# Performance work log

Measured on AMD Instinct MI355X. Metric: run time of the kernel, lower is better.

The kernel has to match this reference:

```python
import jax, jax.numpy as jnp
import numpy as np

EMBED = 512
HEADS = 8
DIM_HEAD = 64
SCALE = DIM_HEAD ** -0.5


def setup_inputs() -> dict:
    key = jax.random.key(0)
    k1, k2, k3 = jax.random.split(key, 3)
    x = jax.random.normal(k1, (1, EMBED, 64, 64), dtype=jnp.float32)
    # nn.Linear(embed, 3*embed) weight [out, in] -> store transposed [in, out] for x @ W
    W_qkv = jax.random.normal(k2, (EMBED, 3 * EMBED), dtype=jnp.float32) * (EMBED ** -0.5)
    b_qkv = jax.random.normal(k3, (3 * EMBED,), dtype=jnp.float32) * 0.01
    return {"x": x, "W_qkv": W_qkv, "b_qkv": b_qkv}


def reference(x, W_qkv, b_qkv):
    B, E, h, w = x.shape
    N = h * w
    # [B, E, H, W] -> [B, N, E]
    xs = x.reshape(B, E, N).transpose(0, 2, 1)
    qkv = xs @ W_qkv + b_qkv                      # [B, N, 3E]
    q, k, v = jnp.split(qkv, 3, axis=-1)          # each [B, N, E]

    def heads(t):
        return t.reshape(B, N, HEADS, DIM_HEAD).transpose(0, 2, 1, 3)  # [B, H, N, dh]

    q, k, v = heads(q), heads(k), heads(v)
    # raw (non-softmax) attention scores, materialized as in the original
    attn = jnp.einsum('bhqd,bhkd->bhqk', q, k) * SCALE  # [B, H, N, N]
    coarse_attn = attn.sum(axis=-2)                     # sum over queries -> [B, H, N]
    output = jnp.einsum('bhqk,bhkd->bhqd', attn, v)     # [B, H, N, dh]
    return coarse_attn, output
```

## Files before the change

### kernel.cpp

```cpp
#include <hip/hip_runtime.h>


#define N_TOK 4096
#define EMBED 512
#define J3    1536
#define HEADS 8
#define DH    64
#define SCALE 0.125f

typedef float  floatx4  __attribute__((ext_vector_type(4)));
typedef short  shortx8  __attribute__((ext_vector_type(8)));
typedef unsigned short ushortx4 __attribute__((ext_vector_type(4)));
typedef unsigned int u32;
typedef unsigned short ushort;

__device__ inline ushort f2bf(float f) {
    union { float f; u32 u; } x; x.f = f;
    u32 r = x.u + 0x7fffu + ((x.u >> 16) & 1u);
    return (ushort)(r >> 16);
}
__device__ inline float bf2f(ushort u) {
    union { u32 u; float f; } x; x.u = ((u32)u) << 16; return x.f;
}
__device__ static inline void async_copy16(void* lds, const void* g) {
    auto* gp = (const __attribute__((address_space(1))) u32*)g;
    auto* lp = (__attribute__((address_space(3))) u32*)lds;
    __builtin_amdgcn_global_load_lds(gp, lp, 16, 0, 0);
}
__device__ inline int permj(int j) {
    if (j < 512) return j;
    if (j < 1024) return 512 + ((j - 512) >> 6) * 128 + ((j - 512) & 63);
    return 512 + ((j - 1024) >> 6) * 128 + 64 + ((j - 1024) & 63);
}

__global__ __launch_bounds__(256) void prep(const float* __restrict__ x,
                                            const float* __restrict__ W,
                                            ushort* __restrict__ xT,
                                            ushort* __restrict__ WT,
                                            float* __restrict__ xsum) {
    const int t = threadIdx.x;
    int bx = blockIdx.x;
    const bool isx = bx < 64;
    const float* src = isx ? x : W;
    const int C = isx ? N_TOK : J3;
    if (!isx) bx -= 64;
    __shared__ float T[64][65];
    __shared__ float red[256];
    const int c0 = bx * 64, r0 = blockIdx.y * 64;
    #pragma unroll
    for (int k = 0; k < 16; ++k) {
        int i = t + 256 * k; int r = i >> 6, c = i & 63;
        T[r][c] = src[(size_t)(r0 + r) * C + c0 + c];
    }
    __syncthreads();
    if (isx) {
        int row = t >> 2, seg = (t & 3) * 16;
        float s = 0.f;
        #pragma unroll
        for (int cc = 0; cc < 16; ++cc) s += T[row][seg + cc];
        red[t] = s;
    }
    #pragma unroll
    for (int k = 0; k < 4; ++k) {
        int i = t + 256 * k; int cr = i >> 4, cc4 = (i & 15) * 4;
        ushortx4 o = { f2bf(T[cc4 + 0][cr]), f2bf(T[cc4 + 1][cr]),
                       f2bf(T[cc4 + 2][cr]), f2bf(T[cc4 + 3][cr]) };
        int dr = isx ? (c0 + cr) : permj(c0 + cr);
        ushort* dst = isx ? xT : WT;
        *(ushortx4*)&dst[(size_t)dr * 512 + r0 + cc4] = o;
    }
    if (isx) {
        __syncthreads();
        if ((t & 3) == 0)
            atomicAdd(&xsum[r0 + (t >> 2)], red[t] + red[t + 1] + red[t + 2] + red[t + 3]);
    }
}

__global__ __launch_bounds__(256) void qkv_m(const ushort* __restrict__ xT,
                                             const ushort* __restrict__ WT,
                                             const float* __restrict__ bias,
                                             ushort* __restrict__ qkv,
                                             float* __restrict__ Mp) {
    const int bx = blockIdx.x, ch = blockIdx.y;
    const int j0 = bx * 128, n0 = ch * 128;
    const bool iskv = bx >= 4;
    const int h = bx - 4;
    __shared__ __align__(16) char lds[34816];
    short* As = (short*)lds;
    short* Bs = (short*)(lds + 8192);
    short* Kt = (short*)lds;
    short* Vt = (short*)(lds + 17408);
    const int t = threadIdx.x, lane = t & 63, w = t >> 6;
    const int wm = w & 1, wn = w >> 1;
    const int quad = lane >> 4, mrow = lane & 15;
    floatx4 acc[4][4] = {};
    for (int e0 = 0; e0 < 512; e0 += 32) {
        __syncthreads();
        #pragma unroll
        for (int s = 0; s < 2; ++s) {
            int i = t + 256 * s; int row = i >> 2, q = i & 3;
            async_copy16((char*)As + (size_t)w * 1024 + (size_t)s * 4096,
                         xT + (size_t)(n0 + row) * 512 + e0 + q * 8);
            async_copy16((char*)Bs + (size_t)w * 1024 + (size_t)s * 4096,
                         WT + (size_t)(j0 + row) * 512 + e0 + q * 8);
        }
        __syncthreads();
        shortx8 a[4], b[4];
        #pragma unroll
        for (int mi = 0; mi < 4; ++mi)
            a[mi] = *(const shortx8*)&As[(wm * 64 + mi * 16 + mrow) * 32 + quad * 8];
        #pragma unroll
        for (int ni = 0; ni < 4; ++ni)
            b[ni] = *(const shortx8*)&Bs[(wn * 64 + ni * 16 + mrow) * 32 + quad * 8];
        #pragma unroll
        for (int mi = 0; mi < 4; ++mi)
            #pragma unroll
            for (int ni = 0; ni < 4; ++ni)
                acc[mi][ni] = __builtin_amdgcn_mfma_f32_16x16x32_bf16(a[mi], b[ni], acc[mi][ni], 0, 0, 0);
    }
    __syncthreads();
    {
        short* ldst = (wn == 0) ? Kt : Vt;
        #pragma unroll
        for (int ni = 0; ni < 4; ++ni) {
            int cl = wn * 64 + ni * 16 + mrow;
            float bj;
            if (!iskv) bj = bias[j0 + cl];
            else bj = (cl < 64) ? bias[512 + h * 64 + cl] : bias[1024 + h * 64 + cl - 64];
            int dh = ni * 16 + mrow;
            #pragma unroll
            for (int mi = 0; mi < 4; ++mi)
                #pragma unroll
                for (int r = 0; r < 4; ++r) {
                    int tok = wm * 64 + mi * 16 + quad * 4 + r;
                    float v = acc[mi][ni][r] + bj;
                    ushort bf = f2bf(v);
                    if (!iskv) {
                        qkv[(size_t)(n0 + tok) * J3 + j0 + cl] = bf;
                    } else {
                        ldst[dh * 136 + tok] = (short)bf;
                        if (cl < 64)
                            qkv[(size_t)(n0 + tok) * J3 + 512 + h * 128 + cl] = bf;
                    }
                }
        }
    }
    if (!iskv) return;
    __syncthreads();
    const int dpb = (w & 1) * 32, db = (w >> 1) * 32;
    floatx4 m[2][2] = {};
    #pragma unroll
    for (int kt = 0; kt < 4; ++kt) {
        shortx8 ka[2], vb[2];
        #pragma unroll
        for (int fi = 0; fi < 2; ++fi)
            ka[fi] = *(const shortx8*)&Kt[(dpb + fi * 16 + mrow) * 136 + kt * 32 + quad * 8];
        #pragma unroll
        for (int fj = 0; fj < 2; ++fj)
            vb[fj] = *(const shortx8*)&Vt[(db + fj * 16 + mrow) * 136 + kt * 32 + quad * 8];
        #pragma unroll
        for (int fi = 0; fi < 2; ++fi)
            #pragma unroll
            for (int fj = 0; fj < 2; ++fj)
                m[fi][fj] = __builtin_amdgcn_mfma_f32_16x16x32_bf16(ka[fi], vb[fj], m[fi][fj], 0, 0, 0);
    }
    float* mp = Mp + ((size_t)h * 32 + ch) * 4096;
    #pragma unroll
    for (int fi = 0; fi < 2; ++fi)
        #pragma unroll
        for (int fj = 0; fj < 2; ++fj)
            #pragma unroll
            for (int r = 0; r < 4; ++r)
                mp[(dpb + fi * 16 + quad * 4 + r) * 64 + db + fj * 16 + mrow] = m[fi][fj][r];
}

__global__ __launch_bounds__(256) void reduce_qm(const float* __restrict__ Mp,
                                                 const ushort* __restrict__ WT,
                                                 const float* __restrict__ bias,
                                                 const float* __restrict__ xsum,
                                                 ushort* __restrict__ Mt,
                                                 float* __restrict__ qsum) {
    const int h = blockIdx.x, part = blockIdx.y;
    const int t = threadIdx.x;
    __shared__ float Msh[16][68];
    __shared__ float red[256];
    const int i0 = part * 1024 + t * 4;
    floatx4 s = {0.f, 0.f, 0.f, 0.f};
    #pragma unroll 4
    for (int c = 0; c < 32; ++c)
        s += *(const floatx4*)&Mp[((size_t)h * 32 + c) * 4096 + i0];
    const int dpl = t >> 4, d0 = (t & 15) * 4;
    *(floatx4*)&Msh[dpl][d0] = s;
    __syncthreads();
    {
        int d = t >> 2, dpl0 = (t & 3) * 4;
        ushortx4 o = { f2bf(Msh[dpl0 + 0][d]), f2bf(Msh[dpl0 + 1][d]),
                       f2bf(Msh[dpl0 + 2][d]), f2bf(Msh[dpl0 + 3][d]) };
        *(ushortx4*)&Mt[(size_t)h * 4096 + d * 64 + part * 16 + dpl0] = o;
    }
    {
        int row = t >> 4, seg = (t & 15) * 32;
        int j = h * 64 + part * 16 + row;
        float qa = 0.f;
        #pragma unroll
        for (int g = 0; g < 4; ++g) {
            shortx8 wv = *(const shortx8*)(WT + (size_t)j * 512 + seg + g * 8);
            #pragma unroll
            for (int u = 0; u < 8; ++u)
                qa += bf2f((ushort)wv[u]) * xsum[seg + g * 8 + u];
        }
        red[t] = qa;
    }
    __syncthreads();
    if (t < 16) {
        float tot = 0.f;
        #pragma unroll
        for (int g = 0; g < 16; ++g) tot += red[t * 16 + g];
        int j = h * 64 + part * 16 + t;
        qsum[j] = 4096.f * bias[j] + tot;
    }
}

__global__ __launch_bounds__(64) void out_kernel(const ushort* __restrict__ qkv,
                                                 const ushort* __restrict__ Mt,
                                                 const float* __restrict__ qsum,
                                                 float* __restrict__ out) {
    const int h = blockIdx.x, n0 = blockIdx.y * 64;
    const int lane = threadIdx.x;
    const int quad = lane >> 4, mrow = lane & 15;
    floatx4 acc[4][4] = {};
    #pragma unroll
    for (int ks = 0; ks < 2; ++ks) {
        shortx8 a[4], b[4];
        #pragma unroll
        for (int mi = 0; mi < 4; ++mi)
            a[mi] = *(const shortx8*)(qkv + (size_t)(n0 + mi * 16 + mrow) * J3 + h * DH + ks * 32 + quad * 8);
        #pragma unroll
        for (int ni = 0; ni < 4; ++ni)
            b[ni] = *(const shortx8*)(Mt + (size_t)h * 4096 + (ni * 16 + mrow) * 64 + ks * 32 + quad * 8);
        #pragma unroll
        for (int mi = 0; mi < 4; ++mi)
            #pragma unroll
            for (int ni = 0; ni < 4; ++ni)
                acc[mi][ni] = __builtin_amdgcn_mfma_f32_16x16x32_bf16(a[mi], b[ni], acc[mi][ni], 0, 0, 0);
    }
    float* op = out + HEADS * N_TOK + (size_t)h * N_TOK * DH;
    #pragma unroll
    for (int mi = 0; mi < 4; ++mi)
        #pragma unroll
        for (int r = 0; r < 4; ++r) {
            int n = n0 + mi * 16 + quad * 4 + r;
            #pragma unroll
            for (int ni = 0; ni < 4; ++ni)
                op[(size_t)n * DH + ni * 16 + mrow] = acc[mi][ni][r] * SCALE;
        }
    float ca = 0.f;
    #pragma unroll
    for (int g = 0; g < 8; ++g) {
        shortx8 kk = *(const shortx8*)(qkv + (size_t)(n0 + lane) * J3 + 512 + h * 128 + g * 8);
        #pragma unroll
        for (int j = 0; j < 8; ++j)
            ca += bf2f((ushort)kk[j]) * qsum[h * DH + g * 8 + j];
    }
    out[h * N_TOK + n0 + lane] = ca * SCALE;
}

extern "C" void kernel_launch(void* const* d_in, const int* in_sizes, int n_in,
                              void* d_out, int out_size, void* d_ws, size_t ws_size,
                              hipStream_t stream) {
    const float* x = (const float*)d_in[0];
    const float* W = (const float*)d_in[1];
    const float* b = (const float*)d_in[2];
    float* out = (float*)d_out;

    ushort* xT = (ushort*)d_ws;
    ushort* WT = xT + (size_t)N_TOK * EMBED;
    ushort* qkvb = WT + (size_t)J3 * EMBED;
    ushort* Mt = qkvb + (size_t)N_TOK * J3;
    float* Mp   = (float*)(Mt + (size_t)HEADS * DH * DH);
    float* xsum = Mp + (size_t)HEADS * 32 * 4096;
    float* qsum = xsum + 512;

    prep<<<dim3(88, 8), 256, 0, stream>>>(x, W, xT, WT, xsum);
    qkv_m<<<dim3(12, 32), 256, 0, stream>>>(xT, WT, b, qkvb, Mp);
    reduce_qm<<<dim3(8, 4), 256, 0, stream>>>(Mp, WT, b, xsum, Mt, qsum);
    out_kernel<<<dim3(8, 64), 64, 0, stream>>>(qkvb, Mt, qsum, out);
}
```

Before: 99.33 us.

## Fold K^T V and Q weights into one projection matrix applied to x

The Q projection is no longer materialised. Per head, the code builds P = W_q · (K^T V) · scale, plus a row for the coarse-attention term, into a 576x512 matrix PT. Both outputs then come from one GEMM of xT against PT, with bias terms added through rbuf. The KV kernel now uses 64-token chunks, which doubles the grid, and the qkv buffer write is gone. The cost is a split hi/lo bf16 product to keep precision, an extra non-transposed bf16 copy of W, and an extra rounding step when P is cast to bf16.

```diff
diff --git a/kernel.cpp b/kernel.cpp
--- a/kernel.cpp
+++ b/kernel.cpp
@@ -37,6 +37,7 @@
                                             const float* __restrict__ W,
                                             ushort* __restrict__ xT,
                                             ushort* __restrict__ WT,
+                                            ushort* __restrict__ Wb,
                                             float* __restrict__ xsum) {
     const int t = threadIdx.x;
     int bx = blockIdx.x;
@@ -69,6 +70,15 @@
         ushort* dst = isx ? xT : WT;
         *(ushortx4*)&dst[(size_t)dr * 512 + r0 + cc4] = o;
     }
+    if (!isx) {
+        #pragma unroll
+        for (int k = 0; k < 4; ++k) {
+            int i = t + 256 * k; int rr = i >> 4, c4 = (i & 15) * 4;
+            ushortx4 o = { f2bf(T[rr][c4 + 0]), f2bf(T[rr][c4 + 1]),
+                           f2bf(T[rr][c4 + 2]), f2bf(T[rr][c4 + 3]) };
+            *(ushortx4*)&Wb[(size_t)(r0 + rr) * J3 + c0 + c4] = o;
+        }
+    }
     if (isx) {
         __syncthreads();
         if ((t & 3) == 0)
@@ -76,44 +86,37 @@
     }
 }
 
-__global__ __launch_bounds__(256) void qkv_m(const ushort* __restrict__ xT,
-                                             const ushort* __restrict__ WT,
-                                             const float* __restrict__ bias,
-                                             ushort* __restrict__ qkv,
-                                             float* __restrict__ Mp) {
-    const int bx = blockIdx.x, ch = blockIdx.y;
-    const int j0 = bx * 128, n0 = ch * 128;
-    const bool iskv = bx >= 4;
-    const int h = bx - 4;
-    __shared__ __align__(16) char lds[34816];
+__global__ __launch_bounds__(256) void kv_m(const ushort* __restrict__ xT,
+                                            const ushort* __restrict__ WT,
+                                            const float* __restrict__ bias,
+                                            float* __restrict__ Mp) {
+    const int h = blockIdx.x, ch = blockIdx.y;
+    const int j0 = 512 + h * 128, n0 = ch * 64;
+    __shared__ __align__(16) char lds[18432];
     short* As = (short*)lds;
-    short* Bs = (short*)(lds + 8192);
+    short* Bs = (short*)(lds + 4096);
     short* Kt = (short*)lds;
-    short* Vt = (short*)(lds + 17408);
+    short* Vt = (short*)(lds + 9216);
     const int t = threadIdx.x, lane = t & 63, w = t >> 6;
     const int wm = w & 1, wn = w >> 1;
     const int quad = lane >> 4, mrow = lane & 15;
-    floatx4 acc[4][4] = {};
+    const int rowA = t >> 2, qa = t & 3;
+    floatx4 acc[2][4] = {};
     for (int e0 = 0; e0 < 512; e0 += 32) {
         __syncthreads();
-        #pragma unroll
-        for (int s = 0; s < 2; ++s) {
-            int i = t + 256 * s; int row = i >> 2, q = i & 3;
-            async_copy16((char*)As + (size_t)w * 1024 + (size_t)s * 4096,
-                         xT + (size_t)(n0 + row) * 512 + e0 + q * 8);
-            async_copy16((char*)Bs + (size_t)w * 1024 + (size_t)s * 4096,
-                         WT + (size_t)(j0 + row) * 512 + e0 + q * 8);
-        }
+        async_copy16((char*)As + (size_t)w * 1024,        xT + (size_t)(n0 + rowA) * 512 + e0 + qa * 8);
+        async_copy16((char*)Bs + (size_t)w * 1024,        WT + (size_t)(j0 + rowA) * 512 + e0 + qa * 8);
+        async_copy16((char*)Bs + 4096 + (size_t)w * 1024, WT + (size_t)(j0 + 64 + rowA) * 512 + e0 + qa * 8);
         __syncthreads();
-        shortx8 a[4], b[4];
-        #pragma unroll
-        for (int mi = 0; mi < 4; ++mi)
-            a[mi] = *(const shortx8*)&As[(wm * 64 + mi * 16 + mrow) * 32 + quad * 8];
+        shortx8 a[2], b[4];
+        #pragma unroll
+        for (int mi = 0; mi < 2; ++mi)
+            a[mi] = *(const shortx8*)&As[(wm * 32 + mi * 16 + mrow) * 32 + quad * 8];
         #pragma unroll
         for (int ni = 0; ni < 4; ++ni)
             b[ni] = *(const shortx8*)&Bs[(wn * 64 + ni * 16 + mrow) * 32 + quad * 8];
         #pragma unroll
-        for (int mi = 0; mi < 4; ++mi)
+        for (int mi = 0; mi < 2; ++mi)
             #pragma unroll
             for (int ni = 0; ni < 4; ++ni)
                 acc[mi][ni] = __builtin_amdgcn_mfma_f32_16x16x32_bf16(a[mi], b[ni], acc[mi][ni], 0, 0, 0);
@@ -124,145 +127,190 @@
         #pragma unroll
         for (int ni = 0; ni < 4; ++ni) {
             int cl = wn * 64 + ni * 16 + mrow;
-            float bj;
-            if (!iskv) bj = bias[j0 + cl];
-            else bj = (cl < 64) ? bias[512 + h * 64 + cl] : bias[1024 + h * 64 + cl - 64];
+            float bj = (cl < 64) ? bias[512 + h * 64 + cl] : bias[1024 + h * 64 + cl - 64];
             int dh = ni * 16 + mrow;
             #pragma unroll
-            for (int mi = 0; mi < 4; ++mi)
+            for (int mi = 0; mi < 2; ++mi)
                 #pragma unroll
-                for (int r = 0; r < 4; ++r) {
-                    int tok = wm * 64 + mi * 16 + quad * 4 + r;
-                    float v = acc[mi][ni][r] + bj;
-                    ushort bf = f2bf(v);
-                    if (!iskv) {
-                        qkv[(size_t)(n0 + tok) * J3 + j0 + cl] = bf;
-                    } else {
-                        ldst[dh * 136 + tok] = (short)bf;
-                        if (cl < 64)
-                            qkv[(size_t)(n0 + tok) * J3 + 512 + h * 128 + cl] = bf;
-                    }
+                for (int rr = 0; rr < 4; ++rr) {
+                    int tok = wm * 32 + mi * 16 + quad * 4 + rr;
+                    ldst[dh * 72 + tok] = (short)f2bf(acc[mi][ni][rr] + bj);
                 }
         }
     }
-    if (!iskv) return;
     __syncthreads();
     const int dpb = (w & 1) * 32, db = (w >> 1) * 32;
     floatx4 m[2][2] = {};
     #pragma unroll
-    for (int kt = 0; kt < 4; ++kt) {
+    for (int kt = 0; kt < 2; ++kt) {
         shortx8 ka[2], vb[2];
         #pragma unroll
         for (int fi = 0; fi < 2; ++fi)
-            ka[fi] = *(const shortx8*)&Kt[(dpb + fi * 16 + mrow) * 136 + kt * 32 + quad * 8];
+            ka[fi] = *(const shortx8*)&Kt[(dpb + fi * 16 + mrow) * 72 + kt * 32 + quad * 8];
         #pragma unroll
         for (int fj = 0; fj < 2; ++fj)
-            vb[fj] = *(const shortx8*)&Vt[(db + fj * 16 + mrow) * 136 + kt * 32 + quad * 8];
+            vb[fj] = *(const shortx8*)&Vt[(db + fj * 16 + mrow) * 72 + kt * 32 + quad * 8];
         #pragma unroll
         for (int fi = 0; fi < 2; ++fi)
             #pragma unroll
             for (int fj = 0; fj < 2; ++fj)
                 m[fi][fj] = __builtin_amdgcn_mfma_f32_16x16x32_bf16(ka[fi], vb[fj], m[fi][fj], 0, 0, 0);
     }
-    float* mp = Mp + ((size_t)h * 32 + ch) * 4096;
+    float* mp = Mp + ((size_t)h * 64 + ch) * 4096;
     #pragma unroll
     for (int fi = 0; fi < 2; ++fi)
         #pragma unroll
         for (int fj = 0; fj < 2; ++fj)
             #pragma unroll
-            for (int r = 0; r < 4; ++r)
-                mp[(dpb + fi * 16 + quad * 4 + r) * 64 + db + fj * 16 + mrow] = m[fi][fj][r];
-}
-
-__global__ __launch_bounds__(256) void reduce_qm(const float* __restrict__ Mp,
-                                                 const ushort* __restrict__ WT,
-                                                 const float* __restrict__ bias,
-                                                 const float* __restrict__ xsum,
-                                                 ushort* __restrict__ Mt,
-                                                 float* __restrict__ qsum) {
+            for (int rr = 0; rr < 4; ++rr)
+                mp[(dpb + fi * 16 + quad * 4 + rr) * 64 + db + fj * 16 + mrow] = m[fi][fj][rr];
+}
+
+__global__ __launch_bounds__(256) void reduce_build(const float* __restrict__ Mp,
+                                                    const ushort* __restrict__ WT,
+                                                    const ushort* __restrict__ Wb,
+                                                    const float* __restrict__ bias,
+                                                    const float* __restrict__ xsum,
+                                                    ushort* __restrict__ PT,
+                                                    float* __restrict__ rbuf) {
     const int h = blockIdx.x, part = blockIdx.y;
     const int t = threadIdx.x;
-    __shared__ float Msh[16][68];
+    const int dv0 = part * 16;
+    __shared__ float Msub[64][17];
     __shared__ float red[256];
-    const int i0 = part * 1024 + t * 4;
-    floatx4 s = {0.f, 0.f, 0.f, 0.f};
+    __shared__ float Qs[64];
+    {
+        int dp = t >> 2, g = t & 3;
+        floatx4 s = {0.f, 0.f, 0.f, 0.f};
+        #pragma unroll 8
+        for (int c = 0; c < 64; ++c)
+            s += *(const floatx4*)&Mp[((size_t)(h * 64 + c)) * 4096 + dp * 64 + dv0 + g * 4];
+        Msub[dp][g * 4 + 0] = s[0]; Msub[dp][g * 4 + 1] = s[1];
+        Msub[dp][g * 4 + 2] = s[2]; Msub[dp][g * 4 + 3] = s[3];
+    }
+    {
+        int jl = t >> 2, sg = t & 3;
+        const ushort* wrow = WT + (size_t)(h * 64 + jl) * 512 + sg * 128;
+        float qa = 0.f;
+        #pragma unroll
+        for (int g = 0; g < 16; ++g) {
+            shortx8 wv = *(const shortx8*)(wrow + g * 8);
+            #pragma unroll
+            for (int u = 0; u < 8; ++u)
+                qa += bf2f((ushort)wv[u]) * xsum[sg * 128 + g * 8 + u];
+        }
+        red[t] = qa;
+    }
+    __syncthreads();
+    if (t < 64) Qs[t] = 4096.f * bias[h * 64 + t] + red[t * 4] + red[t * 4 + 1] + red[t * 4 + 2] + red[t * 4 + 3];
+    {
+        const int lane = t & 63, w = t >> 6;
+        const int quad = lane >> 4, mrow = lane & 15;
+        const int we0 = w * 128;
+        floatx4 acc[8] = {};
+        #pragma unroll
+        for (int ks = 0; ks < 2; ++ks) {
+            shortx8 ahi, alo;
+            #pragma unroll
+            for (int kq = 0; kq < 8; ++kq) {
+                int dk = ks * 32 + quad * 8 + kq;
+                float v = SCALE * Msub[dk][mrow];
+                ushort hi = f2bf(v);
+                ahi[kq] = (short)hi;
+                alo[kq] = (short)f2bf(v - bf2f(hi));
+            }
+            #pragma unroll
+            for (int ni = 0; ni < 8; ++ni) {
+                shortx8 b = *(const shortx8*)(Wb + (size_t)(we0 + ni * 16 + mrow) * J3 + h * 64 + ks * 32 + quad * 8);
+                acc[ni] = __builtin_amdgcn_mfma_f32_16x16x32_bf16(ahi, b, acc[ni], 0, 0, 0);
+                acc[ni] = __builtin_amdgcn_mfma_f32_16x16x32_bf16(alo, b, acc[ni], 0, 0, 0);
+            }
+        }
+        #pragma unroll
+        for (int ni = 0; ni < 8; ++ni)
+            #pragma unroll
+            for (int rr = 0; rr < 4; ++rr)
+                PT[(size_t)(h * 64 + dv0 + quad * 4 + rr) * 512 + we0 + ni * 16 + mrow] = f2bf(acc[ni][rr]);
+    }
+    if (t < 16) {
+        float s = 0.f;
+        #pragma unroll
+        for (int dk = 0; dk < 64; ++dk) s += bias[h * 64 + dk] * Msub[dk][t];
+        rbuf[h * 64 + dv0 + t] = SCALE * s;
+    }
+    __syncthreads();
+    if (part == 0) {
+        for (int e = t; e < 512; e += 256) {
+            float s = 0.f;
+            #pragma unroll
+            for (int g = 0; g < 8; ++g) {
+                shortx8 wv = *(const shortx8*)(Wb + (size_t)e * J3 + 512 + h * 64 + g * 8);
+                #pragma unroll
+                for (int u = 0; u < 8; ++u) s += bf2f((ushort)wv[u]) * Qs[g * 8 + u];
+            }
+            PT[(size_t)(512 + h) * 512 + e] = f2bf(SCALE * s);
+        }
+        if (t == 0) {
+            float s = 0.f;
+            #pragma unroll
+            for (int dk = 0; dk < 64; ++dk) s += bias[512 + h * 64 + dk] * Qs[dk];
+            rbuf[512 + h] = SCALE * s;
+        }
+    }
+    {
+        int idx = h * 4 + part;
+        #pragma unroll
+        for (int z = 0; z < 2; ++z) {
+            int row = 520 + idx * 2 + z;
+            if (row < 576) {
+                PT[(size_t)row * 512 + t] = 0;
+                PT[(size_t)row * 512 + 256 + t] = 0;
+                if (t == 0) rbuf[row] = 0.f;
+            }
+        }
+    }
+}
+
+__global__ __launch_bounds__(256) void outf(const ushort* __restrict__ xT,
+                                            const ushort* __restrict__ PT,
+                                            const float* __restrict__ rbuf,
+                                            float* __restrict__ out) {
+    const int c0 = blockIdx.x * 64, n0 = blockIdx.y * 64;
+    const int t = threadIdx.x, lane = t & 63, w = t >> 6;
+    const int wm = w & 1, wn = w >> 1;
+    const int quad = lane >> 4, mrow = lane & 15;
+    const ushort* pa0 = xT + (size_t)(n0 + wm * 32 + mrow) * 512 + quad * 8;
+    const ushort* pa1 = pa0 + 16 * 512;
+    const ushort* pb0 = PT + (size_t)(c0 + wn * 32 + mrow) * 512 + quad * 8;
+    const ushort* pb1 = pb0 + 16 * 512;
+    floatx4 acc[2][2] = {};
     #pragma unroll 4
-    for (int c = 0; c < 32; ++c)
-        s += *(const floatx4*)&Mp[((size_t)h * 32 + c) * 4096 + i0];
-    const int dpl = t >> 4, d0 = (t & 15) * 4;
-    *(floatx4*)&Msh[dpl][d0] = s;
-    __syncthreads();
-    {
-        int d = t >> 2, dpl0 = (t & 3) * 4;
-        ushortx4 o = { f2bf(Msh[dpl0 + 0][d]), f2bf(Msh[dpl0 + 1][d]),
-                       f2bf(Msh[dpl0 + 2][d]), f2bf(Msh[dpl0 + 3][d]) };
-        *(ushortx4*)&Mt[(size_t)h * 4096 + d * 64 + part * 16 + dpl0] = o;
-    }
-    {
-        int row = t >> 4, seg = (t & 15) * 32;
-        int j = h * 64 + part * 16 + row;
-        float qa = 0.f;
-        #pragma unroll
-        for (int g = 0; g < 4; ++g) {
-            shortx8 wv = *(const shortx8*)(WT + (size_t)j * 512 + seg + g * 8);
-            #pragma unroll
-            for (int u = 0; u < 8; ++u)
-                qa += bf2f((ushort)wv[u]) * xsum[seg + g * 8 + u];
-        }
-        red[t] = qa;
-    }
-    __syncthreads();
-    if (t < 16) {
-        float tot = 0.f;
-        #pragma unroll
-        for (int g = 0; g < 16; ++g) tot += red[t * 16 + g];
-        int j = h * 64 + part * 16 + t;
-        qsum[j] = 4096.f * bias[j] + tot;
-    }
-}
-
-__global__ __launch_bounds__(64) void out_kernel(const ushort* __restrict__ qkv,
-                                                 const ushort* __restrict__ Mt,
-                                                 const float* __restrict__ qsum,
-                                                 float* __restrict__ out) {
-    const int h = blockIdx.x, n0 = blockIdx.y * 64;
-    const int lane = threadIdx.x;
-    const int quad = lane >> 4, mrow = lane & 15;
-    floatx4 acc[4][4] = {};
-    #pragma unroll
-    for (int ks = 0; ks < 2; ++ks) {
-        shortx8 a[4], b[4];
-        #pragma unroll
-        for (int mi = 0; mi < 4; ++mi)
-            a[mi] = *(const shortx8*)(qkv + (size_t)(n0 + mi * 16 + mrow) * J3 + h * DH + ks * 32 + quad * 8);
-        #pragma unroll
-        for (int ni = 0; ni < 4; ++ni)
-            b[ni] = *(const shortx8*)(Mt + (size_t)h * 4096 + (ni * 16 + mrow) * 64 + ks * 32 + quad * 8);
-        #pragma unroll
-        for (int mi = 0; mi < 4; ++mi)
-            #pragma unroll
-            for (int ni = 0; ni < 4; ++ni)
-                acc[mi][ni] = __builtin_amdgcn_mfma_f32_16x16x32_bf16(a[mi], b[ni], acc[mi][ni], 0, 0, 0);
-    }
-    float* op = out + HEADS * N_TOK + (size_t)h * N_TOK * DH;
-    #pragma unroll
-    for (int mi = 0; mi < 4; ++mi)
-        #pragma unroll
-        for (int r = 0; r < 4; ++r) {
-            int n = n0 + mi * 16 + quad * 4 + r;
-            #pragma unroll
-            for (int ni = 0; ni < 4; ++ni)
-                op[(size_t)n * DH + ni * 16 + mrow] = acc[mi][ni][r] * SCALE;
-        }
-    float ca = 0.f;
-    #pragma unroll
-    for (int g = 0; g < 8; ++g) {
-        shortx8 kk = *(const shortx8*)(qkv + (size_t)(n0 + lane) * J3 + 512 + h * 128 + g * 8);
-        #pragma unroll
-        for (int j = 0; j < 8; ++j)
-            ca += bf2f((ushort)kk[j]) * qsum[h * DH + g * 8 + j];
-    }
-    out[h * N_TOK + n0 + lane] = ca * SCALE;
+    for (int e0 = 0; e0 < 512; e0 += 32) {
+        shortx8 a0 = *(const shortx8*)(pa0 + e0);
+        shortx8 a1 = *(const shortx8*)(pa1 + e0);
+        shortx8 b0 = *(const shortx8*)(pb0 + e0);
+        shortx8 b1 = *(const shortx8*)(pb1 + e0);
+        acc[0][0] = __builtin_amdgcn_mfma_f32_16x16x32_bf16(a0, b0, acc[0][0], 0, 0, 0);
+        acc[0][1] = __builtin_amdgcn_mfma_f32_16x16x32_bf16(a0, b1, acc[0][1], 0, 0, 0);
+        acc[1][0] = __builtin_amdgcn_mfma_f32_16x16x32_bf16(a1, b0, acc[1][0], 0, 0, 0);
+        acc[1][1] = __builtin_amdgcn_mfma_f32_16x16x32_bf16(a1, b1, acc[1][1], 0, 0, 0);
+    }
+    #pragma unroll
+    for (int ni = 0; ni < 2; ++ni) {
+        int c = c0 + wn * 32 + ni * 16 + mrow;
+        float rc = rbuf[c];
+        #pragma unroll
+        for (int mi = 0; mi < 2; ++mi)
+            #pragma unroll
+            for (int rr = 0; rr < 4; ++rr) {
+                int n = n0 + wm * 32 + mi * 16 + quad * 4 + rr;
+                float val = acc[mi][ni][rr] + rc;
+                if (c < 512)
+                    out[32768 + (size_t)(c >> 6) * 262144 + (size_t)n * 64 + (c & 63)] = val;
+                else if (c < 520)
+                    out[(size_t)(c - 512) * 4096 + n] = val;
+            }
+    }
 }
 
 extern "C" void kernel_launch(void* const* d_in, const int* in_sizes, int n_in,
@@ -275,14 +323,14 @@
 
     ushort* xT = (ushort*)d_ws;
     ushort* WT = xT + (size_t)N_TOK * EMBED;
-    ushort* qkvb = WT + (size_t)J3 * EMBED;
-    ushort* Mt = qkvb + (size_t)N_TOK * J3;
-    float* Mp   = (float*)(Mt + (size_t)HEADS * DH * DH);
-    float* xsum = Mp + (size_t)HEADS * 32 * 4096;
-    float* qsum = xsum + 512;
-
-    prep<<<dim3(88, 8), 256, 0, stream>>>(x, W, xT, WT, xsum);
-    qkv_m<<<dim3(12, 32), 256, 0, stream>>>(xT, WT, b, qkvb, Mp);
-    reduce_qm<<<dim3(8, 4), 256, 0, stream>>>(Mp, WT, b, xsum, Mt, qsum);
-    out_kernel<<<dim3(8, 64), 64, 0, stream>>>(qkvb, Mt, qsum, out);
-}
+    ushort* Wb = WT + (size_t)J3 * EMBED;
+    ushort* PT = Wb + (size_t)EMBED * J3;
+    float*  Mp = (float*)(PT + (size_t)576 * 512);
+    float* xsum = Mp + (size_t)HEADS * 64 * 4096;
+    float* rbuf = xsum + 512;
+
+    prep<<<dim3(88, 8), 256, 0, stream>>>(x, W, xT, WT, Wb, xsum);
+    kv_m<<<dim3(8, 64), 256, 0, stream>>>(xT, WT, b, Mp);
+    reduce_build<<<dim3(8, 4), 256, 0, stream>>>(Mp, WT, Wb, b, xsum, PT, rbuf);
+    outf<<<dim3(9, 64), 256, 0, stream>>>(xT, PT, rbuf, out);
+}
```

New measurement: 121.8 us. 22.6% more time.
